# Kernel tuning notes

Measured on AMD Instinct MI355X. Metric: run time of the kernel, lower is better.

Reference implementation:

```python
import jax, jax.numpy as jnp
import numpy as np

D_MODEL = 1024
NUM_HEADS = 16
D_HEAD = D_MODEL // NUM_HEADS
B, S = 4, 2048


def setup_inputs() -> dict:
    key = jax.random.key(0)
    ks = jax.random.split(key, 9)
    scale = 1.0 / np.sqrt(D_MODEL)
    inp = {
        "x": jax.random.normal(ks[0], (B, S, D_MODEL), dtype=jnp.float32),
        "mask": jnp.ones((1, 1, S, S), dtype=jnp.int32),
        "Wq": jax.random.normal(ks[1], (D_MODEL, D_MODEL), dtype=jnp.float32) * scale,
        "bq": jax.random.normal(ks[2], (D_MODEL,), dtype=jnp.float32) * scale,
        "Wk": jax.random.normal(ks[3], (D_MODEL, D_MODEL), dtype=jnp.float32) * scale,
        "bk": jax.random.normal(ks[4], (D_MODEL,), dtype=jnp.float32) * scale,
        "Wv": jax.random.normal(ks[5], (D_MODEL, D_MODEL), dtype=jnp.float32) * scale,
        "bv": jax.random.normal(ks[6], (D_MODEL,), dtype=jnp.float32) * scale,
        "Wo": jax.random.normal(ks[7], (D_MODEL, D_MODEL), dtype=jnp.float32) * scale,
        "bo": jax.random.normal(ks[8], (D_MODEL,), dtype=jnp.float32) * scale,
    }
    return inp


def reference(x, mask, Wq, bq, Wk, bk, Wv, bv, Wo, bo):
    b, s, _ = x.shape
    # torch nn.Linear: y = x @ W.T + b
    def split_heads(t):
        return t.reshape(b, s, NUM_HEADS, D_HEAD).transpose(0, 2, 1, 3)  # [b,h,s,dh]
    Q = split_heads(x @ Wq.T + bq)
    K = split_heads(x @ Wk.T + bk)
    V = split_heads(x @ Wv.T + bv)
    scores = jnp.einsum("bhqd,bhkd->bhqk", Q, K) / jnp.sqrt(jnp.float32(D_HEAD))
    scores = jnp.where(mask == 0, jnp.float32(-jnp.inf), scores)
    attn = jax.nn.softmax(scores, axis=-1)
    out = jnp.einsum("bhqk,bhkd->bhqd", attn, V)  # [b,h,s,dh]
    out = out.transpose(0, 2, 1, 3).reshape(b, s, D_MODEL)
    return out @ Wo.T + bo
```

## Files before the change

### kernel.cpp

```cpp
#include <hip/hip_runtime.h>

typedef _Float16 half8 __attribute__((ext_vector_type(8)));
typedef _Float16 half4v __attribute__((ext_vector_type(4)));
typedef __fp16 fp16x2 __attribute__((ext_vector_type(2)));
typedef float f32x4 __attribute__((ext_vector_type(4)));
typedef float f32x16 __attribute__((ext_vector_type(16)));

__device__ __forceinline__ void gld_lds16(const void* g, void* l) {
  __builtin_amdgcn_global_load_lds((const __attribute__((address_space(1))) void*)g,
                                   (__attribute__((address_space(3))) void*)l, 16, 0, 0);
}

__device__ __forceinline__ float fexp2(float x) { return __builtin_amdgcn_exp2f(x); }

__device__ __forceinline__ unsigned pku(float a, float b) {
  union { fp16x2 p; unsigned u; } u;
  u.p = __builtin_amdgcn_cvt_pkrtz(a, b);
  return u.u;
}
__device__ __forceinline__ half4v pk4(float a, float b, float c, float d) {
  union { fp16x2 p[2]; half4v v; } u;
  u.p[0] = __builtin_amdgcn_cvt_pkrtz(a, b);
  u.p[1] = __builtin_amdgcn_cvt_pkrtz(c, d);
  return u.v;
}

__global__ void cvt_f32_f16(const float* __restrict__ src, _Float16* __restrict__ dst, int n4) {
  int i = blockIdx.x * 256 + threadIdx.x;
  if (i < n4) {
    float4 v = ((const float4*)src)[i];
    half4v h;
    h.x = (_Float16)v.x; h.y = (_Float16)v.y; h.z = (_Float16)v.z; h.w = (_Float16)v.w;
    ((half4v*)dst)[i] = h;
  }
}

__global__ void cvt_w4(const float* __restrict__ Wq, const float* __restrict__ Wk,
                       const float* __restrict__ Wv, const float* __restrict__ Wo,
                       _Float16* __restrict__ Wqkv, _Float16* __restrict__ Woh) {
  int i = blockIdx.x * 256 + threadIdx.x;
  int which = i >> 18;
  int local = i & 262143;
  const float* src = which == 0 ? Wq : which == 1 ? Wk : which == 2 ? Wv : Wo;
  float4 v = ((const float4*)src)[local];
  half4v h;
  h.x = (_Float16)v.x; h.y = (_Float16)v.y; h.z = (_Float16)v.z; h.w = (_Float16)v.w;
  _Float16* dst = which < 3 ? Wqkv + (size_t)which * 1048576 : Woh;
  ((half4v*)dst)[local] = h;
}

__global__ void mask_flags_k(const int* __restrict__ mask, unsigned char* __restrict__ flags) {
  int qt = blockIdx.x, kt = blockIdx.y;
  __shared__ int allv;
  if (threadIdx.x == 0) allv = 1;
  __syncthreads();
  int ok = 1;
  for (int idx = threadIdx.x; idx < 128 * 64; idx += 256) {
    int qr = qt * 128 + (idx >> 6);
    int kc = kt * 64 + (idx & 63);
    ok &= (mask[(size_t)qr * 2048 + kc] != 0);
  }
  if (!ok) atomicAnd(&allv, 0);
  __syncthreads();
  if (threadIdx.x == 0) flags[qt * 32 + kt] = (unsigned char)allv;
}

__global__ __launch_bounds__(256, 2) void gemm_qkv(const _Float16* __restrict__ A,
                                                   const _Float16* __restrict__ B,
                                                   const float* __restrict__ bq,
                                                   const float* __restrict__ bk,
                                                   const float* __restrict__ bv,
                                                   _Float16* __restrict__ Qw,
                                                   _Float16* __restrict__ Kw,
                                                   _Float16* __restrict__ Vtt,
                                                   float qscale) {
  __shared__ _Float16 Alds[128][32];
  __shared__ _Float16 Blds[128][32];
  int tid = threadIdx.x, w = tid >> 6, l = tid & 63;
  int lm = l & 15, lg = l >> 4;
  int wm = w >> 1, wn = w & 1;
  int wg = blockIdx.y * 24 + blockIdx.x;
  int xcd = wg & 7, j = wg >> 3;
  int panel = j >> 6, rem = j & 63;
  int m0 = (xcd * 8 + (rem >> 3)) * 128;
  int n0 = (panel * 8 + (rem & 7)) * 128;
  f32x4 acc[4][4] = {};
  for (int k0 = 0; k0 < 1024; k0 += 32) {
#pragma unroll
    for (int c = 0; c < 2; ++c) {
      int o = w * 2048 + c * 1024 + l * 16;
      int row = o >> 6;
      int kb = (o & 63) >> 1;
      gld_lds16(A + (size_t)(m0 + row) * 1024 + k0 + kb, (char*)&Alds[0][0] + w * 2048 + c * 1024);
      gld_lds16(B + (size_t)(n0 + row) * 1024 + k0 + kb, (char*)&Blds[0][0] + w * 2048 + c * 1024);
    }
    __syncthreads();
    half8 af[4], bf[4];
#pragma unroll
    for (int m = 0; m < 4; ++m) af[m] = *(const half8*)&Alds[wm * 64 + m * 16 + lm][lg * 8];
#pragma unroll
    for (int n = 0; n < 4; ++n) bf[n] = *(const half8*)&Blds[wn * 64 + n * 16 + lm][lg * 8];
#pragma unroll
    for (int m = 0; m < 4; ++m)
#pragma unroll
      for (int n = 0; n < 4; ++n)
        acc[m][n] = __builtin_amdgcn_mfma_f32_16x16x32_f16(af[m], bf[n], acc[m][n], 0, 0, 0);
    __syncthreads();
  }
  int which = n0 >> 10;
  float osc = which == 0 ? qscale : 1.0f;
  const float* bias = which == 0 ? bq : which == 1 ? bk : bv;
  int cq0 = n0 & 1023;
  float bs[4];
#pragma unroll
  for (int n = 0; n < 4; ++n) bs[n] = bias[cq0 + wn * 64 + n * 16 + lm];
#pragma unroll
  for (int m = 0; m < 4; ++m) {
#pragma unroll
    for (int n = 0; n < 4; ++n) {
      int cq = cq0 + wn * 64 + n * 16 + lm;
      int hh = cq >> 6, d = cq & 63;
#pragma unroll
      for (int j2 = 0; j2 < 4; ++j2) {
        int rowg = m0 + wm * 64 + m * 16 + lg * 4 + j2;
        int b = rowg >> 11, s = rowg & 2047;
        float v = (acc[m][n][j2] + bs[n]) * osc;
        if (which == 2) {
          Vtt[((size_t)(b * 16 + hh) * 64 + d) * 2048 + s] = (_Float16)v;
        } else {
          _Float16* dst = which == 0 ? Qw : Kw;
          dst[((size_t)(b * 16 + hh) * 2048 + s) * 64 + d] = (_Float16)v;
        }
      }
    }
  }
}

__global__ __launch_bounds__(256, 2) void gemm_o(const _Float16* __restrict__ A,
                                                 const _Float16* __restrict__ B,
                                                 const float* __restrict__ bias,
                                                 float* __restrict__ dst) {
  __shared__ _Float16 Alds[128][32];
  __shared__ _Float16 Blds[128][32];
  int tid = threadIdx.x, w = tid >> 6, l = tid & 63;
  int lm = l & 15, lg = l >> 4;
  int wm = w >> 1, wn = w & 1;
  int wg = blockIdx.y * 8 + blockIdx.x;
  int xcd = wg & 7, j = wg >> 3;
  int m0 = (xcd * 8 + (j >> 3)) * 128, n0 = (j & 7) * 128;
  f32x4 acc[4][4] = {};
  for (int k0 = 0; k0 < 1024; k0 += 32) {
#pragma unroll
    for (int c = 0; c < 2; ++c) {
      int o = w * 2048 + c * 1024 + l * 16;
      int row = o >> 6;
      int kb = (o & 63) >> 1;
      gld_lds16(A + (size_t)(m0 + row) * 1024 + k0 + kb, (char*)&Alds[0][0] + w * 2048 + c * 1024);
      gld_lds16(B + (size_t)(n0 + row) * 1024 + k0 + kb, (char*)&Blds[0][0] + w * 2048 + c * 1024);
    }
    __syncthreads();
    half8 af[4], bf[4];
#pragma unroll
    for (int m = 0; m < 4; ++m) af[m] = *(const half8*)&Alds[wm * 64 + m * 16 + lm][lg * 8];
#pragma unroll
    for (int n = 0; n < 4; ++n) bf[n] = *(const half8*)&Blds[wn * 64 + n * 16 + lm][lg * 8];
#pragma unroll
    for (int m = 0; m < 4; ++m)
#pragma unroll
      for (int n = 0; n < 4; ++n)
        acc[m][n] = __builtin_amdgcn_mfma_f32_16x16x32_f16(af[m], bf[n], acc[m][n], 0, 0, 0);
    __syncthreads();
  }
  float bs[4];
#pragma unroll
  for (int n = 0; n < 4; ++n) bs[n] = bias[n0 + wn * 64 + n * 16 + lm];
#pragma unroll
  for (int m = 0; m < 4; ++m)
#pragma unroll
    for (int n = 0; n < 4; ++n) {
      int colg = n0 + wn * 64 + n * 16 + lm;
#pragma unroll
      for (int j2 = 0; j2 < 4; ++j2) {
        int rowg = m0 + wm * 64 + m * 16 + lg * 4 + j2;
        dst[(size_t)rowg * 1024 + colg] = acc[m][n][j2] + bs[n];
      }
    }
}

__global__ __launch_bounds__(256) void attn_k(const _Float16* __restrict__ Q,
                                              const _Float16* __restrict__ K,
                                              const _Float16* __restrict__ Vt,
                                              const unsigned char* __restrict__ flags,
                                              const int* __restrict__ mask,
                                              _Float16* __restrict__ out) {
  __shared__ __align__(16) char lds[2][16384];
  int bh = blockIdx.x, qt = blockIdx.y;
  int tid = threadIdx.x, w = tid >> 6, l = tid & 63;
  int c = l & 31, h = l >> 5;
  const size_t hb = (size_t)bh * (2048 * 64);
  int q0 = qt * 128 + w * 32;
  const _Float16* Kb = K + hb;
  const _Float16* Vb = Vt + hb;
  const unsigned char* fl = flags + qt * 32;

  int sr = (l >> 3), scb = (l & 7) * 16;

  half8 qf[4];
#pragma unroll
  for (int ds = 0; ds < 4; ++ds)
    qf[ds] = *(const half8*)&Q[hb + (size_t)(q0 + c) * 64 + ds * 16 + h * 8];

  f32x16 oaccT[2] = {};
  float mrun = -1e30f;
  float lrun = 0.f;

#pragma unroll
  for (int i = 0; i < 2; ++i) {
    int r = w * 16 + i * 8 + sr;
    int dk = (scb ^ ((r & 7) << 4)) >> 1;
    gld_lds16(Kb + (size_t)r * 64 + dk, &lds[0][(w * 16 + i * 8) * 128]);
    gld_lds16(Vb + (size_t)r * 2048 + dk, &lds[0][8192 + (w * 16 + i * 8) * 128]);
  }
  __syncthreads();
  int buf = 0;

  for (int t = 0; t < 32; ++t) {
    if (t < 31) {
#pragma unroll
      for (int i = 0; i < 2; ++i) {
        int r = w * 16 + i * 8 + sr;
        int dk = (scb ^ ((r & 7) << 4)) >> 1;
        gld_lds16(Kb + (size_t)((t + 1) * 64 + r) * 64 + dk,
                  &lds[buf ^ 1][(w * 16 + i * 8) * 128]);
        gld_lds16(Vb + (size_t)r * 2048 + (t + 1) * 64 + dk,
                  &lds[buf ^ 1][8192 + (w * 16 + i * 8) * 128]);
      }
    }
    int flg = fl[t];
    f32x16 sT[2];
    f32x16 z = {};
    __builtin_amdgcn_s_setprio(1);
#pragma unroll
    for (int n = 0; n < 2; ++n) {
      int kr = n * 32 + c;
#pragma unroll
      for (int ds = 0; ds < 4; ++ds) {
        half8 kf = *(const half8*)&lds[buf][kr * 128 + ((ds * 32 + h * 16) ^ ((kr & 7) << 4))];
        sT[n] = ds == 0 ? __builtin_amdgcn_mfma_f32_32x32x16_f16(kf, qf[0], z, 0, 0, 0)
                        : __builtin_amdgcn_mfma_f32_32x32x16_f16(kf, qf[ds], sT[n], 0, 0, 0);
      }
    }
    __builtin_amdgcn_s_setprio(0);
    if (!flg) {
#pragma unroll
      for (int n = 0; n < 2; ++n)
#pragma unroll
        for (int r = 0; r < 16; ++r) {
          int kc = t * 64 + n * 32 + (r & 3) + 8 * (r >> 2) + 4 * h;
          if (mask[(size_t)(q0 + c) * 2048 + kc] == 0) sT[n][r] = -1e30f;
        }
    }
    float mx[16];
#pragma unroll
    for (int r = 0; r < 16; ++r) mx[r] = fmaxf(sT[0][r], sT[1][r]);
#pragma unroll
    for (int step = 8; step >= 1; step >>= 1)
#pragma unroll
      for (int r = 0; r < 8; ++r)
        if (r < step) mx[r] = fmaxf(mx[r], mx[r + step]);
    float pmax = mx[0];
    pmax = fmaxf(pmax, __shfl_xor(pmax, 32, 64));
    if (!__all(pmax - mrun <= 8.f)) {
      float mnew = fmaxf(mrun, pmax);
      float alpha = fexp2(mrun - mnew);
#pragma unroll
      for (int dh = 0; dh < 2; ++dh)
#pragma unroll
        for (int r = 0; r < 16; ++r) oaccT[dh][r] *= alpha;
      lrun *= alpha;
      mrun = mnew;
    }
    unsigned pk_[2][8];
    float psum = 0.f;
#pragma unroll
    for (int n = 0; n < 2; ++n)
#pragma unroll
      for (int g = 0; g < 4; ++g) {
        float p0 = fexp2(sT[n][4 * g + 0] - mrun);
        float p1 = fexp2(sT[n][4 * g + 1] - mrun);
        float p2 = fexp2(sT[n][4 * g + 2] - mrun);
        float p3 = fexp2(sT[n][4 * g + 3] - mrun);
        psum += (p0 + p1) + (p2 + p3);
        pk_[n][2 * g] = pku(p0, p1);
        pk_[n][2 * g + 1] = pku(p2, p3);
      }
    lrun += psum;
    __builtin_amdgcn_s_setprio(1);
#pragma unroll
    for (int n = 0; n < 2; ++n)
#pragma unroll
      for (int sp = 0; sp < 2; ++sp) {
        unsigned a0 = pk_[n][4 * sp], a1 = pk_[n][4 * sp + 1];
        unsigned b0 = pk_[n][4 * sp + 2], b1 = pk_[n][4 * sp + 3];
        unsigned sa0 = (unsigned)__shfl_xor((int)a0, 32, 64);
        unsigned sa1 = (unsigned)__shfl_xor((int)a1, 32, 64);
        unsigned sb0 = (unsigned)__shfl_xor((int)b0, 32, 64);
        unsigned sb1 = (unsigned)__shfl_xor((int)b1, 32, 64);
        union { unsigned u[4]; half8 v; } pb;
        pb.u[0] = h ? sb0 : a0;
        pb.u[1] = h ? sb1 : a1;
        pb.u[2] = h ? b0 : sa0;
        pb.u[3] = h ? b1 : sa1;
        int s = n * 2 + sp;
#pragma unroll
        for (int dh = 0; dh < 2; ++dh) {
          int vr = dh * 32 + c;
          half8 vfr = *(const half8*)&lds[buf][8192 + vr * 128 + ((s * 32 + h * 16) ^ ((vr & 7) << 4))];
          oaccT[dh] = __builtin_amdgcn_mfma_f32_32x32x16_f16(vfr, pb.v, oaccT[dh], 0, 0, 0);
        }
      }
    __builtin_amdgcn_s_setprio(0);
    __syncthreads();
    buf ^= 1;
  }
  char* Pl = &lds[0][w * 4096];
  int bb = bh >> 4, hh = bh & 15;
  float lsum = lrun + __shfl_xor(lrun, 32, 64);
  float rinv = 1.0f / lsum;
#pragma unroll
  for (int dh = 0; dh < 2; ++dh)
#pragma unroll
    for (int g = 0; g < 4; ++g) {
      int dbase = dh * 32 + 8 * g + 4 * h;
      int byte = c * 128 + ((dbase * 2) ^ ((c & 7) << 4));
      *(half4v*)(&Pl[byte]) = pk4(oaccT[dh][4 * g + 0] * rinv, oaccT[dh][4 * g + 1] * rinv,
                                  oaccT[dh][4 * g + 2] * rinv, oaccT[dh][4 * g + 3] * rinv);
    }
#pragma unroll
  for (int r = 0; r < 4; ++r) {
    int o = r * 1024 + l * 16;
    int row = o >> 7;
    int pb_ = o & 127;
    int d2 = pb_ ^ ((row & 7) << 4);
    half8 v = *(const half8*)&Pl[row * 128 + pb_];
    *(half8*)&out[((size_t)(bb * 2048 + q0 + row)) * 1024 + hh * 64 + (d2 >> 1)] = v;
  }
}

extern "C" void kernel_launch(void* const* d_in, const int* in_sizes, int n_in,
                              void* d_out, int out_size, void* d_ws, size_t ws_size,
                              hipStream_t stream) {
  const float* x = (const float*)d_in[0];
  const int* mask = (const int*)d_in[1];
  const float* Wq = (const float*)d_in[2];
  const float* bq = (const float*)d_in[3];
  const float* Wk = (const float*)d_in[4];
  const float* bk = (const float*)d_in[5];
  const float* Wv = (const float*)d_in[6];
  const float* bv = (const float*)d_in[7];
  const float* Wo = (const float*)d_in[8];
  const float* bo = (const float*)d_in[9];

  char* ws = (char*)d_ws;
  _Float16* xh = (_Float16*)(ws);
  _Float16* Wqkvh = (_Float16*)(ws + (16ull << 20));
  _Float16* Woh = (_Float16*)(ws + (22ull << 20));
  _Float16* Vt = (_Float16*)(ws + (24ull << 20));
  unsigned char* flags = (unsigned char*)(ws + (40ull << 20));
  _Float16* Qw = (_Float16*)d_out;
  _Float16* Kw = (_Float16*)((char*)d_out + (16ull << 20));
  _Float16* Ah = xh;

  const float QSCALE = 0.125f * 1.4426950408889634f;

  cvt_f32_f16<<<8192, 256, 0, stream>>>(x, xh, 2097152);
  cvt_w4<<<4096, 256, 0, stream>>>(Wq, Wk, Wv, Wo, Wqkvh, Woh);
  mask_flags_k<<<dim3(16, 32), 256, 0, stream>>>(mask, flags);
  gemm_qkv<<<dim3(24, 64), 256, 0, stream>>>(xh, Wqkvh, bq, bk, bv, Qw, Kw, Vt, QSCALE);
  attn_k<<<dim3(64, 16), 256, 0, stream>>>(Qw, Kw, Vt, flags, mask, Ah);
  gemm_o<<<dim3(8, 64), 256, 0, stream>>>(Ah, Woh, bo, (float*)d_out);
}
```

Baseline: 250.7 us.

## Double-buffer LDS tiles in QKV and output GEMMs with MFMA priority boost

Both projection GEMMs now keep two LDS buffers per operand. The next K-slice is issued through global_load_lds before the MFMAs run on the current slice, which removes one barrier per iteration and overlaps global-to-LDS traffic with matrix math. s_setprio raises wave priority around the MFMA block, and the minimum-blocks hint is dropped from launch_bounds. The trade-off is twice the LDS per block and a possible change in occupancy and register allocation.

```diff
diff --git a/kernel.cpp b/kernel.cpp
--- a/kernel.cpp
+++ b/kernel.cpp
@@ -65,17 +65,27 @@
   if (threadIdx.x == 0) flags[qt * 32 + kt] = (unsigned char)allv;
 }
 
-__global__ __launch_bounds__(256, 2) void gemm_qkv(const _Float16* __restrict__ A,
-                                                   const _Float16* __restrict__ B,
-                                                   const float* __restrict__ bq,
-                                                   const float* __restrict__ bk,
-                                                   const float* __restrict__ bv,
-                                                   _Float16* __restrict__ Qw,
-                                                   _Float16* __restrict__ Kw,
-                                                   _Float16* __restrict__ Vtt,
-                                                   float qscale) {
-  __shared__ _Float16 Alds[128][32];
-  __shared__ _Float16 Blds[128][32];
+#define STAGE_TILE(DST, SRC, base0, kk0)                                         \
+  _Pragma("unroll")                                                              \
+  for (int cc = 0; cc < 2; ++cc) {                                               \
+    int oo = w * 2048 + cc * 1024 + l * 16;                                      \
+    int row_ = oo >> 6;                                                          \
+    int kb_ = (oo & 63) >> 1;                                                    \
+    gld_lds16(SRC + (size_t)((base0) + row_) * 1024 + (kk0) + kb_,               \
+              (char*)&DST[0][0] + w * 2048 + cc * 1024);                         \
+  }
+
+__global__ __launch_bounds__(256) void gemm_qkv(const _Float16* __restrict__ A,
+                                                const _Float16* __restrict__ B,
+                                                const float* __restrict__ bq,
+                                                const float* __restrict__ bk,
+                                                const float* __restrict__ bv,
+                                                _Float16* __restrict__ Qw,
+                                                _Float16* __restrict__ Kw,
+                                                _Float16* __restrict__ Vtt,
+                                                float qscale) {
+  __shared__ _Float16 Alds[2][128][32];
+  __shared__ _Float16 Blds[2][128][32];
   int tid = threadIdx.x, w = tid >> 6, l = tid & 63;
   int lm = l & 15, lg = l >> 4;
   int wm = w >> 1, wn = w & 1;
@@ -85,27 +95,29 @@
   int m0 = (xcd * 8 + (rem >> 3)) * 128;
   int n0 = (panel * 8 + (rem & 7)) * 128;
   f32x4 acc[4][4] = {};
+  STAGE_TILE(Alds[0], A, m0, 0);
+  STAGE_TILE(Blds[0], B, n0, 0);
+  __syncthreads();
+  int buf = 0;
   for (int k0 = 0; k0 < 1024; k0 += 32) {
-#pragma unroll
-    for (int c = 0; c < 2; ++c) {
-      int o = w * 2048 + c * 1024 + l * 16;
-      int row = o >> 6;
-      int kb = (o & 63) >> 1;
-      gld_lds16(A + (size_t)(m0 + row) * 1024 + k0 + kb, (char*)&Alds[0][0] + w * 2048 + c * 1024);
-      gld_lds16(B + (size_t)(n0 + row) * 1024 + k0 + kb, (char*)&Blds[0][0] + w * 2048 + c * 1024);
-    }
-    __syncthreads();
+    if (k0 < 992) {
+      STAGE_TILE(Alds[buf ^ 1], A, m0, k0 + 32);
+      STAGE_TILE(Blds[buf ^ 1], B, n0, k0 + 32);
+    }
     half8 af[4], bf[4];
 #pragma unroll
-    for (int m = 0; m < 4; ++m) af[m] = *(const half8*)&Alds[wm * 64 + m * 16 + lm][lg * 8];
-#pragma unroll
-    for (int n = 0; n < 4; ++n) bf[n] = *(const half8*)&Blds[wn * 64 + n * 16 + lm][lg * 8];
+    for (int m = 0; m < 4; ++m) af[m] = *(const half8*)&Alds[buf][wm * 64 + m * 16 + lm][lg * 8];
+#pragma unroll
+    for (int n = 0; n < 4; ++n) bf[n] = *(const half8*)&Blds[buf][wn * 64 + n * 16 + lm][lg * 8];
+    __builtin_amdgcn_s_setprio(1);
 #pragma unroll
     for (int m = 0; m < 4; ++m)
 #pragma unroll
       for (int n = 0; n < 4; ++n)
         acc[m][n] = __builtin_amdgcn_mfma_f32_16x16x32_f16(af[m], bf[n], acc[m][n], 0, 0, 0);
+    __builtin_amdgcn_s_setprio(0);
     __syncthreads();
+    buf ^= 1;
   }
   int which = n0 >> 10;
   float osc = which == 0 ? qscale : 1.0f;
@@ -136,12 +148,12 @@
   }
 }
 
-__global__ __launch_bounds__(256, 2) void gemm_o(const _Float16* __restrict__ A,
-                                                 const _Float16* __restrict__ B,
-                                                 const float* __restrict__ bias,
-                                                 float* __restrict__ dst) {
-  __shared__ _Float16 Alds[128][32];
-  __shared__ _Float16 Blds[128][32];
+__global__ __launch_bounds__(256) void gemm_o(const _Float16* __restrict__ A,
+                                              const _Float16* __restrict__ B,
+                                              const float* __restrict__ bias,
+                                              float* __restrict__ dst) {
+  __shared__ _Float16 Alds[2][128][32];
+  __shared__ _Float16 Blds[2][128][32];
   int tid = threadIdx.x, w = tid >> 6, l = tid & 63;
   int lm = l & 15, lg = l >> 4;
   int wm = w >> 1, wn = w & 1;
@@ -149,27 +161,29 @@
   int xcd = wg & 7, j = wg >> 3;
   int m0 = (xcd * 8 + (j >> 3)) * 128, n0 = (j & 7) * 128;
   f32x4 acc[4][4] = {};
+  STAGE_TILE(Alds[0], A, m0, 0);
+  STAGE_TILE(Blds[0], B, n0, 0);
+  __syncthreads();
+  int buf = 0;
   for (int k0 = 0; k0 < 1024; k0 += 32) {
-#pragma unroll
-    for (int c = 0; c < 2; ++c) {
-      int o = w * 2048 + c * 1024 + l * 16;
-      int row = o >> 6;
-      int kb = (o & 63) >> 1;
-      gld_lds16(A + (size_t)(m0 + row) * 1024 + k0 + kb, (char*)&Alds[0][0] + w * 2048 + c * 1024);
-      gld_lds16(B + (size_t)(n0 + row) * 1024 + k0 + kb, (char*)&Blds[0][0] + w * 2048 + c * 1024);
-    }
-    __syncthreads();
+    if (k0 < 992) {
+      STAGE_TILE(Alds[buf ^ 1], A, m0, k0 + 32);
+      STAGE_TILE(Blds[buf ^ 1], B, n0, k0 + 32);
+    }
     half8 af[4], bf[4];
 #pragma unroll
-    for (int m = 0; m < 4; ++m) af[m] = *(const half8*)&Alds[wm * 64 + m * 16 + lm][lg * 8];
-#pragma unroll
-    for (int n = 0; n < 4; ++n) bf[n] = *(const half8*)&Blds[wn * 64 + n * 16 + lm][lg * 8];
+    for (int m = 0; m < 4; ++m) af[m] = *(const half8*)&Alds[buf][wm * 64 + m * 16 + lm][lg * 8];
+#pragma unroll
+    for (int n = 0; n < 4; ++n) bf[n] = *(const half8*)&Blds[buf][wn * 64 + n * 16 + lm][lg * 8];
+    __builtin_amdgcn_s_setprio(1);
 #pragma unroll
     for (int m = 0; m < 4; ++m)
 #pragma unroll
       for (int n = 0; n < 4; ++n)
         acc[m][n] = __builtin_amdgcn_mfma_f32_16x16x32_f16(af[m], bf[n], acc[m][n], 0, 0, 0);
+    __builtin_amdgcn_s_setprio(0);
     __syncthreads();
+    buf ^= 1;
   }
   float bs[4];
 #pragma unroll
```

Result: faster. 245.2 us (-2.2%).
